# Kernel optimization log

Measured on AMD Instinct MI355X. Metric: run time of the kernel, lower is better.

## Reference

```python
import jax, jax.numpy as jnp
import numpy as np
import math

B, S, D = 2, 2048, 2048
H = 16
DK = D // H  # 128
DFF = 5440
THETA = 10000.0
EPS = 1e-5


def setup_inputs() -> dict:
    key = jax.random.key(0)
    ks = jax.random.split(key, 9)
    sc = 0.02
    return {
        "x": jax.random.normal(ks[0], (B, S, D), jnp.float32),
        "wq": jax.random.normal(ks[1], (D, D), jnp.float32) * sc,
        "wk": jax.random.normal(ks[2], (D, D), jnp.float32) * sc,
        "wv": jax.random.normal(ks[3], (D, D), jnp.float32) * sc,
        "wo": jax.random.normal(ks[4], (D, D), jnp.float32) * sc,
        "w1": jax.random.normal(ks[5], (DFF, D), jnp.float32) * sc,
        "w2": jax.random.normal(ks[6], (D, DFF), jnp.float32) * sc,
        "w3": jax.random.normal(ks[7], (DFF, D), jnp.float32) * sc,
        "g_attn": jnp.ones((D,), jnp.float32),
        "g_ffn": jnp.ones((D,), jnp.float32),
    }


def _rmsnorm(x, g):
    xf = x.astype(jnp.float32)
    rms = jnp.sqrt(jnp.mean(xf * xf, axis=-1, keepdims=True) + EPS)
    return (xf / rms * g).astype(x.dtype)


def _rope(x):
    # x: (B, H, S, DK)
    pair = jnp.arange(0, DK, 2, dtype=jnp.float32)
    inv_freq = 1.0 / (THETA ** (pair / DK))            # (DK/2,)
    pos = jnp.arange(S, dtype=jnp.float32)
    ang = pos[:, None] * inv_freq[None, :]             # (S, DK/2)
    cos, sin = jnp.cos(ang), jnp.sin(ang)
    xe, xo = x[..., 0::2], x[..., 1::2]
    oe = xe * cos - xo * sin
    oo = xe * sin + xo * cos
    # interleave even/odd back
    out = jnp.stack([oe, oo], axis=-1).reshape(x.shape)
    return out


def reference(x, wq, wk, wv, wo, w1, w2, w3, g_attn, g_ffn):
    # --- attention sublayer ---
    h = _rmsnorm(x, g_attn)
    q = (h @ wq.T).reshape(B, S, H, DK).transpose(0, 2, 1, 3)
    k = (h @ wk.T).reshape(B, S, H, DK).transpose(0, 2, 1, 3)
    v = (h @ wv.T).reshape(B, S, H, DK).transpose(0, 2, 1, 3)
    q = _rope(q)
    k = _rope(k)
    scores = jnp.einsum("bhqd,bhkd->bhqk", q, k) / math.sqrt(DK)
    causal = jnp.tril(jnp.ones((S, S), dtype=bool))
    scores = jnp.where(causal, scores, jnp.finfo(scores.dtype).min)
    attn = jax.nn.softmax(scores, axis=-1)
    o = jnp.einsum("bhqk,bhkd->bhqd", attn, v)
    o = o.transpose(0, 2, 1, 3).reshape(B, S, D)
    x = x + o @ wo.T
    # --- SwiGLU FFN sublayer ---
    h = _rmsnorm(x, g_ffn)
    a = h @ w1.T
    gate = a * jax.nn.sigmoid(a)
    ff = (gate * (h @ w3.T)) @ w2.T
    return x + ff
```

## Files before the change

### kernel.cpp

```cpp
#include <hip/hip_runtime.h>
#include <cstdint>
#include <cstddef>

typedef float  f32x4  __attribute__((ext_vector_type(4)));
typedef __bf16 bf16x8 __attribute__((ext_vector_type(8)));
typedef unsigned short u16x8 __attribute__((ext_vector_type(8)));
typedef unsigned short u16x4 __attribute__((ext_vector_type(4)));
typedef unsigned short u16x2 __attribute__((ext_vector_type(2)));

#define DEV static __device__ __forceinline__

DEV unsigned short f2bfu(float f) { __bf16 b = (__bf16)f; return __builtin_bit_cast(unsigned short, b); }
DEV float bfu2f(unsigned short u) { return (float)__builtin_bit_cast(__bf16, u); }
DEV bf16x8 ldb8(const void* p) { return __builtin_bit_cast(bf16x8, *(const u16x8*)p); }
DEV float fexp(float x) { return __builtin_amdgcn_exp2f(x * 1.44269504f); }

DEV f32x4 mfma16(bf16x8 a, bf16x8 b, f32x4 c) {
  return __builtin_amdgcn_mfma_f32_16x16x32_bf16(a, b, c, 0, 0, 0);
}

DEV void gload16(const void* g, void* l) {
  __builtin_amdgcn_global_load_lds((const unsigned int*)g, (unsigned int*)l, 16, 0, 0);
}

#define FENCE() asm volatile("" ::: "memory")
#define LGKM0() asm volatile("s_waitcnt lgkmcnt(0)" ::: "memory")
#define VMC8()  asm volatile("s_waitcnt vmcnt(8)" ::: "memory")
#define VMC4()  asm volatile("s_waitcnt vmcnt(4)" ::: "memory")
#define VMC0()  asm volatile("s_waitcnt vmcnt(0)" ::: "memory")
#define SBAR()  __builtin_amdgcn_s_barrier()
#define SCH0()  __builtin_amdgcn_sched_barrier(0)
#define PRIO1() __builtin_amdgcn_s_setprio(1)
#define PRIO0() __builtin_amdgcn_s_setprio(0)

__global__ __launch_bounds__(256) void conv_cat3(
    const float* __restrict__ s0, const float* __restrict__ s1,
    const float* __restrict__ s2, unsigned short* __restrict__ d)
{
  size_t i = (size_t)blockIdx.x * 256 + threadIdx.x;
  size_t e = i * 4;
  const float* s = e < 4194304 ? s0 : (e < 8388608 ? s1 : s2);
  f32x4 v = *(const f32x4*)(s + (e & 4194303));
  u16x4 o = { f2bfu(v.x), f2bfu(v.y), f2bfu(v.z), f2bfu(v.w) };
  *(u16x4*)(d + e) = o;
}

__global__ __launch_bounds__(256) void conv_plain(
    const float* __restrict__ s, unsigned short* __restrict__ d)
{
  size_t e = ((size_t)blockIdx.x * 256 + threadIdx.x) * 4;
  f32x4 v = *(const f32x4*)(s + e);
  u16x4 o = { f2bfu(v.x), f2bfu(v.y), f2bfu(v.z), f2bfu(v.w) };
  *(u16x4*)(d + e) = o;
}

__global__ __launch_bounds__(256) void conv_w13(
    const float* __restrict__ w1, const float* __restrict__ w3,
    unsigned short* __restrict__ d)
{
  size_t i = (size_t)blockIdx.x * 256 + threadIdx.x;
  size_t e = i * 4;
  if (e >= 22544384ull) return;
  int n = (int)(e >> 11), kc = (int)(e & 2047);
  int grp = n >> 4;
  int srcrow = (grp >> 1) * 16 + (n & 15);
  if (srcrow >= 5440) srcrow = 5439;
  const float* s = (grp & 1) ? w3 : w1;
  size_t off = (size_t)srcrow * 2048 + kc;
  f32x4 v = *(const f32x4*)(s + off);
  u16x4 o = { f2bfu(v.x), f2bfu(v.y), f2bfu(v.z), f2bfu(v.w) };
  *(u16x4*)(d + e) = o;
}

template<int EPI>
__global__ __launch_bounds__(256) void gemm_p(
    const unsigned short* __restrict__ A, const unsigned short* __restrict__ B,
    void* __restrict__ D0, void* __restrict__ D1, void* __restrict__ D2,
    const float* __restrict__ auxf, const float* __restrict__ cosT,
    const float* __restrict__ sinT, int M, int N, int K)
{
  __shared__ __align__(16) char Asb[4 * 8192];
  __shared__ __align__(16) char Bsb[4 * 8192];

  const int tid = threadIdx.x, lane = tid & 63, w = tid >> 6;
  const int wr = w >> 1, wc = w & 1, l15 = lane & 15, lg = lane >> 4;
  const int m0 = blockIdx.x * 128, n0 = blockIdx.y * 128;

  const int srow = tid >> 2, s4 = tid & 3;
  const int s4s = s4 ^ ((srow >> 1) & 3);
  const unsigned short* As0 = A + (size_t)(m0 + srow) * K + s4s * 8;
  const unsigned short* As1 = A + (size_t)(m0 + 64 + srow) * K + s4s * 8;
  const unsigned short* Bs0 = B + (size_t)(n0 + srow) * K + s4s * 8;
  const unsigned short* Bs1 = B + (size_t)(n0 + 64 + srow) * K + s4s * 8;
  const int dst0 = tid * 16, dst1 = 4096 + tid * 16;

#define STG_A(kh, db, kt) do { char* r = Asb + ((kh)*2+(db))*8192;            \
    gload16(As0 + (size_t)(kt)*64 + (kh)*32, r + dst0);                        \
    gload16(As1 + (size_t)(kt)*64 + (kh)*32, r + dst1); } while(0)
#define STG_B(kh, db, kt) do { char* r = Bsb + ((kh)*2+(db))*8192;            \
    gload16(Bs0 + (size_t)(kt)*64 + (kh)*32, r + dst0);                        \
    gload16(Bs1 + (size_t)(kt)*64 + (kh)*32, r + dst1); } while(0)

  f32x4 zero = {0.f, 0.f, 0.f, 0.f};
  f32x4 acc[4][4];
#pragma unroll
  for (int i = 0; i < 4; i++)
#pragma unroll
    for (int j = 0; j < 4; j++) acc[i][j] = zero;

  int aro[4], bro[4];
#pragma unroll
  for (int mi = 0; mi < 4; mi++) {
    int row = wr * 64 + mi * 16 + l15;
    aro[mi] = row * 64 + ((lg ^ ((row >> 1) & 3)) << 4);
  }
#pragma unroll
  for (int ni = 0; ni < 4; ni++) {
    int row = wc * 64 + ni * 16 + l15;
    bro[ni] = row * 64 + ((lg ^ ((row >> 1) & 3)) << 4);
  }

  const int nkt = K >> 6;

  STG_A(0, 0, 0); STG_B(0, 0, 0); STG_A(1, 0, 0); STG_B(1, 0, 0);

  for (int t = 0; t < nkt; ++t) {
    const int db = t & 1, dn = db ^ 1;
    const bool pf = (t + 1) < nkt;
    const char* Ar0 = Asb + (0 * 2 + db) * 8192;
    const char* Br0 = Bsb + (0 * 2 + db) * 8192;
    const char* Ar1 = Asb + (1 * 2 + db) * 8192;
    const char* Br1 = Bsb + (1 * 2 + db) * 8192;

    VMC4(); FENCE(); SBAR();
    bf16x8 af[4], bfr[4];
#pragma unroll
    for (int ni = 0; ni < 4; ni++) bfr[ni] = ldb8(Br0 + bro[ni]);
#pragma unroll
    for (int mi = 0; mi < 4; mi++) af[mi] = ldb8(Ar0 + aro[mi]);
    if (pf) { STG_A(0, dn, t + 1); STG_B(0, dn, t + 1); }
    LGKM0(); SCH0();
    PRIO1();
#pragma unroll
    for (int mi = 0; mi < 4; mi++)
#pragma unroll
      for (int ni = 0; ni < 4; ni++)
        acc[mi][ni] = mfma16(af[mi], bfr[ni], acc[mi][ni]);
    PRIO0();

    if (pf) { VMC4(); } else { VMC0(); }
    FENCE(); SBAR();
#pragma unroll
    for (int ni = 0; ni < 4; ni++) bfr[ni] = ldb8(Br1 + bro[ni]);
#pragma unroll
    for (int mi = 0; mi < 4; mi++) af[mi] = ldb8(Ar1 + aro[mi]);
    if (pf) { STG_A(1, dn, t + 1); STG_B(1, dn, t + 1); }
    LGKM0(); SCH0();
    PRIO1();
#pragma unroll
    for (int mi = 0; mi < 4; mi++)
#pragma unroll
      for (int ni = 0; ni < 4; ni++)
        acc[mi][ni] = mfma16(af[mi], bfr[ni], acc[mi][ni]);
    PRIO0();
  }
#undef STG_A
#undef STG_B

  if constexpr (EPI == 0) {
    unsigned short* qd = (unsigned short*)D0;
    unsigned short* kd = (unsigned short*)D1;
    unsigned short* vd = (unsigned short*)D2;
#pragma unroll
    for (int mi = 0; mi < 4; mi++) {
#pragma unroll
      for (int ni = 0; ni < 4; ni++) {
        int col = n0 + wc * 64 + ni * 16 + l15;
#pragma unroll
        for (int r = 0; r < 4; r++) {
          int row = m0 + wr * 64 + mi * 16 + lg * 4 + r;
          float v = acc[mi][ni][r];
          if (col < 4096) {
            int d = col & 127, pi = d >> 1, sp = row & 2047;
            float c = cosT[sp * 64 + pi], s = sinT[sp * 64 + pi];
            float part = __shfl_xor(v, 1);
            float res = (d & 1) ? (part * s + v * c) : (v * c - part * s);
            unsigned short* dst = (col < 2048) ? qd : kd;
            dst[(size_t)row * 2048 + (col & 2047)] = f2bfu(res);
          } else {
            int vdc = col - 4096;
            vd[((size_t)((row >> 11) * 2048 + vdc)) * 2048 + (row & 2047)] = f2bfu(v);
          }
        }
      }
    }
  } else {
    float* O = (float*)D0;
#pragma unroll
    for (int mi = 0; mi < 4; mi++)
#pragma unroll
      for (int ni = 0; ni < 4; ni++) {
        int col = n0 + wc * 64 + ni * 16 + l15;
#pragma unroll
        for (int r = 0; r < 4; r++) {
          int row = m0 + wr * 64 + mi * 16 + lg * 4 + r;
          size_t ix = (size_t)row * 2048 + col;
          if constexpr (EPI == 1) O[ix] = auxf[ix] + acc[mi][ni][r];
          else                    O[ix] = O[ix] + acc[mi][ni][r];
        }
      }
  }
}

template<int EPI>
__global__ __launch_bounds__(512, 1) void gemm8v2(
    const unsigned short* __restrict__ A, const unsigned short* __restrict__ B,
    void* __restrict__ D0, int M, int N, int K)
{
  __shared__ __align__(16) char Asb[4 * 16384];
  __shared__ __align__(16) char Bsb[4 * 16384];

  const int tid = threadIdx.x, lane = tid & 63, w = tid >> 6;
  const int wm = w >> 2, wn = w & 3;
  const int l15 = lane & 15, lg = lane >> 4;

  const int nwg = gridDim.x, chunk = nwg >> 3;
  const int wg = (blockIdx.x & 7) * chunk + (blockIdx.x >> 3);
  const int MT = M >> 8;
  const int mt = wg % MT, nt = wg / MT;
  const int m0 = mt * 256, n0 = nt * 256;

  const int srow = tid >> 2;
  const int s4   = tid & 3;
  const int s4s  = s4 ^ ((srow >> 1) & 3);
  const unsigned short* As0 = A + (size_t)(m0 + srow) * K + s4s * 8;
  const unsigned short* As1 = A + (size_t)(m0 + 128 + srow) * K + s4s * 8;
  const unsigned short* Bs0 = B + (size_t)(n0 + srow) * K + s4s * 8;
  const unsigned short* Bs1 = B + (size_t)(n0 + 128 + srow) * K + s4s * 8;
  const int dst0 = tid * 16, dst1 = 8192 + tid * 16;

#define STAGE_A(kh, db, kt) do { char* rgn = Asb + ((kh)*2+(db))*16384;       \
    gload16(As0 + (size_t)(kt)*64 + (kh)*32, rgn + dst0);                      \
    gload16(As1 + (size_t)(kt)*64 + (kh)*32, rgn + dst1); } while(0)
#define STAGE_B(kh, db, kt) do { char* rgn = Bsb + ((kh)*2+(db))*16384;       \
    gload16(Bs0 + (size_t)(kt)*64 + (kh)*32, rgn + dst0);                      \
    gload16(Bs1 + (size_t)(kt)*64 + (kh)*32, rgn + dst1); } while(0)

  f32x4 zero = {0.f, 0.f, 0.f, 0.f};
  f32x4 acc[8][4];
#pragma unroll
  for (int i = 0; i < 8; i++)
#pragma unroll
    for (int j = 0; j < 4; j++) acc[i][j] = zero;

  int aro[8], bro[4];
#pragma unroll
  for (int mi = 0; mi < 8; mi++) {
    int row = wm * 128 + mi * 16 + l15;
    aro[mi] = row * 64 + ((lg ^ ((row >> 1) & 3)) << 4);
  }
#pragma unroll
  for (int ni = 0; ni < 4; ni++) {
    int row = wn * 64 + ni * 16 + l15;
    bro[ni] = row * 64 + ((lg ^ ((row >> 1) & 3)) << 4);
  }

  const int nkt = K >> 6;

  STAGE_A(0, 0, 0); STAGE_B(0, 0, 0); STAGE_A(1, 0, 0); STAGE_B(1, 0, 0);

  for (int t = 0; t < nkt; ++t) {
    const int db = t & 1, dn = db ^ 1;
    const bool pf = (t + 1) < nkt;
    const char* Ar0 = Asb + (0 * 2 + db) * 16384;
    const char* Br0 = Bsb + (0 * 2 + db) * 16384;
    const char* Ar1 = Asb + (1 * 2 + db) * 16384;
    const char* Br1 = Bsb + (1 * 2 + db) * 16384;

    VMC4(); FENCE(); SBAR();
    bf16x8 bfr[4], af[4];
#pragma unroll
    for (int ni = 0; ni < 4; ni++) bfr[ni] = ldb8(Br0 + bro[ni]);
#pragma unroll
    for (int mi = 0; mi < 4; mi++) af[mi] = ldb8(Ar0 + aro[mi]);
    if (pf) STAGE_A(0, dn, t + 1);
    LGKM0(); SCH0();
    PRIO1();
#pragma unroll
    for (int mi = 0; mi < 4; mi++)
#pragma unroll
      for (int ni = 0; ni < 4; ni++)
        acc[mi][ni] = mfma16(af[mi], bfr[ni], acc[mi][ni]);
    PRIO0();

    bf16x8 ag[4];
#pragma unroll
    for (int mi = 0; mi < 4; mi++) ag[mi] = ldb8(Ar0 + aro[mi + 4]);
    if (pf) STAGE_B(0, dn, t + 1);
    LGKM0(); SCH0();
    PRIO1();
#pragma unroll
    for (int mi = 0; mi < 4; mi++)
#pragma unroll
      for (int ni = 0; ni < 4; ni++)
        acc[mi + 4][ni] = mfma16(ag[mi], bfr[ni], acc[mi + 4][ni]);
    PRIO0();

    if (pf) { VMC4(); } else { VMC0(); }
    FENCE(); SBAR();
#pragma unroll
    for (int ni = 0; ni < 4; ni++) bfr[ni] = ldb8(Br1 + bro[ni]);
#pragma unroll
    for (int mi = 0; mi < 4; mi++) af[mi] = ldb8(Ar1 + aro[mi]);
    if (pf) STAGE_A(1, dn, t + 1);
    LGKM0(); SCH0();
    PRIO1();
#pragma unroll
    for (int mi = 0; mi < 4; mi++)
#pragma unroll
      for (int ni = 0; ni < 4; ni++)
        acc[mi][ni] = mfma16(af[mi], bfr[ni], acc[mi][ni]);
    PRIO0();

#pragma unroll
    for (int mi = 0; mi < 4; mi++) ag[mi] = ldb8(Ar1 + aro[mi + 4]);
    if (pf) STAGE_B(1, dn, t + 1);
    LGKM0(); SCH0();
    PRIO1();
#pragma unroll
    for (int mi = 0; mi < 4; mi++)
#pragma unroll
      for (int ni = 0; ni < 4; ni++)
        acc[mi + 4][ni] = mfma16(ag[mi], bfr[ni], acc[mi + 4][ni]);
    PRIO0();
  }
#undef STAGE_A
#undef STAGE_B

  if constexpr (EPI == 2) {
    unsigned short* G = (unsigned short*)D0;
#pragma unroll
    for (int mi = 0; mi < 8; mi++)
#pragma unroll
      for (int nj = 0; nj < 2; nj++) {
        int outc = (nt * 8 + wn * 2 + nj) * 16 + l15;
        if (outc >= 5440) continue;
#pragma unroll
        for (int r = 0; r < 4; r++) {
          int row = m0 + wm * 128 + mi * 16 + lg * 4 + r;
          float a = acc[mi][2 * nj][r];
          float c = acc[mi][2 * nj + 1][r];
          float sg = a / (1.0f + fexp(-a));
          G[(size_t)row * 5440 + outc] = f2bfu(sg * c);
        }
      }
  }
}

__global__ __launch_bounds__(256) void rmsnorm_k(
    const float* __restrict__ x, const float* __restrict__ g,
    unsigned short* __restrict__ out)
{
  int row = blockIdx.x, t = threadIdx.x;
  const float* xr = x + (size_t)row * 2048;
  f32x4 v0 = ((const f32x4*)xr)[t];
  f32x4 v1 = ((const f32x4*)xr)[t + 256];
  float ss = v0.x*v0.x + v0.y*v0.y + v0.z*v0.z + v0.w*v0.w
           + v1.x*v1.x + v1.y*v1.y + v1.z*v1.z + v1.w*v1.w;
  __shared__ float red[256];
  red[t] = ss; __syncthreads();
  for (int sh = 128; sh > 0; sh >>= 1) {
    if (t < sh) red[t] += red[t + sh];
    __syncthreads();
  }
  float rinv = rsqrtf(red[0] * (1.0f / 2048.0f) + 1e-5f);
  f32x4 g0 = ((const f32x4*)g)[t];
  f32x4 g1 = ((const f32x4*)g)[t + 256];
  u16x4 o0 = { f2bfu(v0.x*rinv*g0.x), f2bfu(v0.y*rinv*g0.y),
               f2bfu(v0.z*rinv*g0.z), f2bfu(v0.w*rinv*g0.w) };
  u16x4 o1 = { f2bfu(v1.x*rinv*g1.x), f2bfu(v1.y*rinv*g1.y),
               f2bfu(v1.z*rinv*g1.z), f2bfu(v1.w*rinv*g1.w) };
  *(u16x4*)(out + (size_t)row * 2048 + t * 4) = o0;
  *(u16x4*)(out + (size_t)row * 2048 + 1024 + t * 4) = o1;
}

__global__ __launch_bounds__(256) void rope_tab(float* __restrict__ cosT,
                                                float* __restrict__ sinT)
{
  int idx = blockIdx.x * 256 + threadIdx.x;
  int s = idx >> 6, p = idx & 63;
  float ang = (float)s * powf(10000.0f, -(float)p / 64.0f);
  cosT[idx] = cosf(ang);
  sinT[idx] = sinf(ang);
}

__global__ __launch_bounds__(256) void attn_fwd(
    const unsigned short* __restrict__ q, const unsigned short* __restrict__ k,
    const unsigned short* __restrict__ vt, unsigned short* __restrict__ o)
{
  const int S = 2048, Dm = 2048;
  const int tid  = threadIdx.x;
  const int lane = tid & 63;
  const int w    = tid >> 6;
  const int hh   = blockIdx.y, b = blockIdx.z;
  const int l15  = lane & 15, lg = lane >> 4;
  const float SCALE = 0.08838834764831845f;

  __shared__ __align__(16) char Ksb[2][16384];
  __shared__ __align__(16) char Vsb[2][16384];
  __shared__ __align__(16) unsigned short Ps[4][16 * 76];

  const unsigned short* kg = k  + ((size_t)(b * S)) * Dm + hh * 128;
  const unsigned short* vg = vt + ((size_t)((b * 16 + hh) * 128)) * S;

  const int krs = tid >> 4, ksp = (tid & 15) ^ (krs & 7);
  const int vrs = tid >> 3, vsp = (tid & 7) ^ (vrs & 7);

#define STAGE_KV(j, buf) do {                                                  \
    int kv_ = (j) * 64;                                                        \
    _Pragma("unroll")                                                          \
    for (int rr = 0; rr < 4; rr++)                                             \
      gload16(kg + (size_t)(kv_ + rr * 16 + krs) * 2048 + ksp * 8,             \
              Ksb[buf] + (rr * 256 + tid) * 16);                               \
    _Pragma("unroll")                                                          \
    for (int rr = 0; rr < 4; rr++)                                             \
      gload16(vg + (size_t)(rr * 32 + vrs) * 2048 + kv_ + vsp * 8,             \
              Vsb[buf] + (rr * 256 + tid) * 16);                               \
  } while (0)

  for (int half = 0; half < 2; ++half) {
    const int qt = half ? (31 - blockIdx.x) : blockIdx.x;
    const int r0 = qt * 64;
    const int myq = r0 + w * 16 + l15;

    STAGE_KV(0, 0);

    bf16x8 qf[4];
    size_t qbase = ((size_t)(b * S + r0 + w * 16 + l15)) * Dm + hh * 128 + lg * 8;
#pragma unroll
    for (int kk = 0; kk < 4; kk++) qf[kk] = ldb8(q + qbase + kk * 32);

    f32x4 zero = {0.f, 0.f, 0.f, 0.f};
    f32x4 accO[8];
#pragma unroll
    for (int dt = 0; dt < 8; dt++) accO[dt] = zero;
    float mrun = -1e30f, lrun = 0.f;

    int ntile = qt + 1;
    for (int j = 0; j < ntile; ++j) {
      int kv0 = j * 64;
      const int db = j & 1;
      const bool pf = (j + 1) < ntile;
      if (pf) STAGE_KV(j + 1, db ^ 1);
      if (pf) { VMC8(); } else { VMC0(); }
      FENCE(); SBAR();

      const char* Ks = Ksb[db];
      const char* Vs = Vsb[db];

      f32x4 sfr[4];
#pragma unroll
      for (int sv = 0; sv < 4; sv++) sfr[sv] = zero;
#pragma unroll
      for (int kk = 0; kk < 4; kk++) {
#pragma unroll
        for (int sv = 0; sv < 4; sv++) {
          int row = sv * 16 + l15;
          int boff = (row * 256 + kk * 64 + lg * 16) ^ ((row & 7) << 4);
          bf16x8 kf = ldb8(Ks + boff);
          sfr[sv] = mfma16(kf, qf[kk], sfr[sv]);
        }
      }

      float tmax = -1e30f;
#pragma unroll
      for (int sv = 0; sv < 4; sv++)
#pragma unroll
        for (int r = 0; r < 4; r++) {
          int kvv = kv0 + sv * 16 + lg * 4 + r;
          float val = (kvv <= myq) ? sfr[sv][r] * SCALE : -1e30f;
          sfr[sv][r] = val;
          tmax = fmaxf(tmax, val);
        }
      tmax = fmaxf(tmax, __shfl_xor(tmax, 16));
      tmax = fmaxf(tmax, __shfl_xor(tmax, 32));
      float mnew = fmaxf(mrun, tmax);
      float alpha = fexp(mrun - mnew);
      float psum = 0.f;
#pragma unroll
      for (int sv = 0; sv < 4; sv++)
#pragma unroll
        for (int r = 0; r < 4; r++) {
          float pvv = fexp(sfr[sv][r] - mnew);
          sfr[sv][r] = pvv;
          psum += pvv;
        }
      psum += __shfl_xor(psum, 16);
      psum += __shfl_xor(psum, 32);
      lrun = lrun * alpha + psum;
      mrun = mnew;

      float al[4];
#pragma unroll
      for (int r = 0; r < 4; r++)
        al[r] = __shfl(alpha, (lane & 48) + lg * 4 + r);
#pragma unroll
      for (int dt = 0; dt < 8; dt++) {
        f32x4 t = accO[dt];
        t[0] *= al[0]; t[1] *= al[1]; t[2] *= al[2]; t[3] *= al[3];
        accO[dt] = t;
      }

#pragma unroll
      for (int sv = 0; sv < 4; sv++) {
        u16x2 lo = { f2bfu(sfr[sv][0]), f2bfu(sfr[sv][1]) };
        u16x2 hi = { f2bfu(sfr[sv][2]), f2bfu(sfr[sv][3]) };
        *(u16x2*)&Ps[w][l15 * 76 + sv * 16 + lg * 4]     = lo;
        *(u16x2*)&Ps[w][l15 * 76 + sv * 16 + lg * 4 + 2] = hi;
      }

      bf16x8 pa[2];
      pa[0] = ldb8(&Ps[w][l15 * 76 + lg * 8]);
      pa[1] = ldb8(&Ps[w][l15 * 76 + 32 + lg * 8]);
#pragma unroll
      for (int dt = 0; dt < 8; dt++) {
#pragma unroll
        for (int kk = 0; kk < 2; kk++) {
          int row = dt * 16 + l15;
          int boff = (row * 128 + kk * 64 + lg * 16) ^ ((row & 7) << 4);
          bf16x8 vb = ldb8(Vs + boff);
          accO[dt] = mfma16(pa[kk], vb, accO[dt]);
        }
      }
      FENCE(); SBAR();
    }

    float lf[4];
#pragma unroll
    for (int r = 0; r < 4; r++)
      lf[r] = __shfl(lrun, (lane & 48) + lg * 4 + r);
#pragma unroll
    for (int dt = 0; dt < 8; dt++) {
#pragma unroll
      for (int r = 0; r < 4; r++) {
        int qr = r0 + w * 16 + lg * 4 + r;
        o[((size_t)(b * S + qr)) * Dm + hh * 128 + dt * 16 + l15] =
            f2bfu(accO[dt][r] / lf[r]);
      }
    }
  }
#undef STAGE_KV
}

extern "C" void kernel_launch(void* const* d_in, const int* in_sizes, int n_in,
                              void* d_out, int out_size, void* d_ws, size_t ws_size,
                              hipStream_t stream)
{
  const float* x      = (const float*)d_in[0];
  const float* wq     = (const float*)d_in[1];
  const float* wk     = (const float*)d_in[2];
  const float* wv     = (const float*)d_in[3];
  const float* wo     = (const float*)d_in[4];
  const float* w1     = (const float*)d_in[5];
  const float* w2     = (const float*)d_in[6];
  const float* w3     = (const float*)d_in[7];
  const float* g_attn = (const float*)d_in[8];
  const float* g_ffn  = (const float*)d_in[9];
  float* out = (float*)d_out;

  unsigned short* W = (unsigned short*)d_ws;
  unsigned short* h_bf    = W;
  unsigned short* q_bf    = W + 8388608ull;
  unsigned short* k_bf    = W + 16777216ull;
  unsigned short* vt_bf   = W + 25165824ull;
  unsigned short* o_bf    = W + 33554432ull;
  unsigned short* wqkv_bf = W + 41943040ull;
  unsigned short* wo_bf   = W + 54525952ull;
  unsigned short* w13_bf  = W + 58720256ull;
  unsigned short* w2_bf   = W + 81264640ull;
  unsigned short* a1_bf   = q_bf;
  float* cosT = (float*)o_bf;
  float* sinT = cosT + 131072;

  dim3 blk(256);
  rope_tab<<<512, blk, 0, stream>>>(cosT, sinT);
  conv_cat3<<<12288, blk, 0, stream>>>(wq, wk, wv, wqkv_bf);
  conv_plain<<<4096, blk, 0, stream>>>(wo, wo_bf);
  conv_w13<<<22016, blk, 0, stream>>>(w1, w3, w13_bf);
  conv_plain<<<10880, blk, 0, stream>>>(w2, w2_bf);

  rmsnorm_k<<<4096, blk, 0, stream>>>(x, g_attn, h_bf);

  gemm_p<0><<<dim3(32, 48), blk, 0, stream>>>(h_bf, wqkv_bf, q_bf, k_bf, vt_bf,
                                              nullptr, cosT, sinT, 4096, 6144, 2048);

  attn_fwd<<<dim3(16, 16, 2), blk, 0, stream>>>(q_bf, k_bf, vt_bf, o_bf);

  gemm_p<1><<<dim3(32, 16), blk, 0, stream>>>(o_bf, wo_bf, out, nullptr, nullptr,
                                              x, nullptr, nullptr, 4096, 2048, 2048);
  rmsnorm_k<<<4096, blk, 0, stream>>>(out, g_ffn, h_bf);

  gemm8v2<2><<<dim3(688), dim3(512), 0, stream>>>(h_bf, w13_bf, a1_bf, 4096, 11008, 2048);

  gemm_p<3><<<dim3(32, 16), blk, 0, stream>>>(a1_bf, w2_bf, out, nullptr, nullptr,
                                              nullptr, nullptr, nullptr, 4096, 2048, 5440);
}
```

Measured before the change: 655.9 us.

## Restructure causal attention: 32-key tiles, one q-tile per block, lazy rescale

```diff
diff --git a/kernel.cpp b/kernel.cpp
--- a/kernel.cpp
+++ b/kernel.cpp
@@ -14,6 +14,7 @@
 DEV float bfu2f(unsigned short u) { return (float)__builtin_bit_cast(__bf16, u); }
 DEV bf16x8 ldb8(const void* p) { return __builtin_bit_cast(bf16x8, *(const u16x8*)p); }
 DEV float fexp(float x) { return __builtin_amdgcn_exp2f(x * 1.44269504f); }
+DEV float fexp2(float x) { return __builtin_amdgcn_exp2f(x); }
 
 DEV f32x4 mfma16(bf16x8 a, bf16x8 b, f32x4 c) {
   return __builtin_amdgcn_mfma_f32_16x16x32_bf16(a, b, c, 0, 0, 0);
@@ -25,7 +26,6 @@
 
 #define FENCE() asm volatile("" ::: "memory")
 #define LGKM0() asm volatile("s_waitcnt lgkmcnt(0)" ::: "memory")
-#define VMC8()  asm volatile("s_waitcnt vmcnt(8)" ::: "memory")
 #define VMC4()  asm volatile("s_waitcnt vmcnt(4)" ::: "memory")
 #define VMC0()  asm volatile("s_waitcnt vmcnt(0)" ::: "memory")
 #define SBAR()  __builtin_amdgcn_s_barrier()
@@ -404,102 +404,92 @@
   const int w    = tid >> 6;
   const int hh   = blockIdx.y, b = blockIdx.z;
   const int l15  = lane & 15, lg = lane >> 4;
-  const float SCALE = 0.08838834764831845f;
-
-  __shared__ __align__(16) char Ksb[2][16384];
-  __shared__ __align__(16) char Vsb[2][16384];
-  __shared__ __align__(16) unsigned short Ps[4][16 * 76];
+  const float C = 0.08838834764831845f * 1.44269504f;
+
+  __shared__ __align__(16) char Ksb[2][8192];
+  __shared__ __align__(16) char Vsb[2][8192];
+  __shared__ __align__(16) unsigned short Ps[4][16 * 40];
 
   const unsigned short* kg = k  + ((size_t)(b * S)) * Dm + hh * 128;
   const unsigned short* vg = vt + ((size_t)((b * 16 + hh) * 128)) * S;
 
   const int krs = tid >> 4, ksp = (tid & 15) ^ (krs & 7);
-  const int vrs = tid >> 3, vsp = (tid & 7) ^ (vrs & 7);
+  const int vrs = tid >> 2, vsp = (tid & 3) ^ (vrs & 3);
 
 #define STAGE_KV(j, buf) do {                                                  \
-    int kv_ = (j) * 64;                                                        \
+    int kv_ = (j) * 32;                                                        \
     _Pragma("unroll")                                                          \
-    for (int rr = 0; rr < 4; rr++)                                             \
+    for (int rr = 0; rr < 2; rr++)                                             \
       gload16(kg + (size_t)(kv_ + rr * 16 + krs) * 2048 + ksp * 8,             \
               Ksb[buf] + (rr * 256 + tid) * 16);                               \
     _Pragma("unroll")                                                          \
-    for (int rr = 0; rr < 4; rr++)                                             \
-      gload16(vg + (size_t)(rr * 32 + vrs) * 2048 + kv_ + vsp * 8,             \
+    for (int rr = 0; rr < 2; rr++)                                             \
+      gload16(vg + (size_t)(rr * 64 + vrs) * 2048 + kv_ + vsp * 8,             \
               Vsb[buf] + (rr * 256 + tid) * 16);                               \
   } while (0)
 
-  for (int half = 0; half < 2; ++half) {
-    const int qt = half ? (31 - blockIdx.x) : blockIdx.x;
-    const int r0 = qt * 64;
-    const int myq = r0 + w * 16 + l15;
-
-    STAGE_KV(0, 0);
-
-    bf16x8 qf[4];
-    size_t qbase = ((size_t)(b * S + r0 + w * 16 + l15)) * Dm + hh * 128 + lg * 8;
-#pragma unroll
-    for (int kk = 0; kk < 4; kk++) qf[kk] = ldb8(q + qbase + kk * 32);
-
-    f32x4 zero = {0.f, 0.f, 0.f, 0.f};
-    f32x4 accO[8];
-#pragma unroll
-    for (int dt = 0; dt < 8; dt++) accO[dt] = zero;
-    float mrun = -1e30f, lrun = 0.f;
-
-    int ntile = qt + 1;
-    for (int j = 0; j < ntile; ++j) {
-      int kv0 = j * 64;
-      const int db = j & 1;
-      const bool pf = (j + 1) < ntile;
-      if (pf) STAGE_KV(j + 1, db ^ 1);
-      if (pf) { VMC8(); } else { VMC0(); }
-      FENCE(); SBAR();
-
-      const char* Ks = Ksb[db];
-      const char* Vs = Vsb[db];
-
-      f32x4 sfr[4];
-#pragma unroll
-      for (int sv = 0; sv < 4; sv++) sfr[sv] = zero;
-#pragma unroll
-      for (int kk = 0; kk < 4; kk++) {
-#pragma unroll
-        for (int sv = 0; sv < 4; sv++) {
-          int row = sv * 16 + l15;
-          int boff = (row * 256 + kk * 64 + lg * 16) ^ ((row & 7) << 4);
-          bf16x8 kf = ldb8(Ks + boff);
-          sfr[sv] = mfma16(kf, qf[kk], sfr[sv]);
-        }
+  const int qt = 31 - blockIdx.x;
+  const int r0 = qt * 64;
+  const int myq = r0 + w * 16 + l15;
+
+  STAGE_KV(0, 0);
+
+  bf16x8 qf[4];
+  size_t qbase = ((size_t)(b * S + r0 + w * 16 + l15)) * Dm + hh * 128 + lg * 8;
+#pragma unroll
+  for (int kk = 0; kk < 4; kk++) qf[kk] = ldb8(q + qbase + kk * 32);
+
+  f32x4 zero = {0.f, 0.f, 0.f, 0.f};
+  f32x4 accO[8];
+#pragma unroll
+  for (int dt = 0; dt < 8; dt++) accO[dt] = zero;
+  float mrun = -1e30f, lrun = 0.f;
+
+  const int ntile = 2 * qt + 2;
+  for (int j = 0; j < ntile; ++j) {
+    int kv0 = j * 32;
+    const int db = j & 1;
+    const bool pf = (j + 1) < ntile;
+    if (pf) STAGE_KV(j + 1, db ^ 1);
+    if (pf) { VMC4(); } else { VMC0(); }
+    FENCE(); SBAR();
+
+    const char* Ks = Ksb[db];
+    const char* Vs = Vsb[db];
+
+    f32x4 sfr[2];
+    sfr[0] = zero; sfr[1] = zero;
+    PRIO1();
+#pragma unroll
+    for (int kk = 0; kk < 4; kk++) {
+#pragma unroll
+      for (int sv = 0; sv < 2; sv++) {
+        int row = sv * 16 + l15;
+        int boff = (row * 256 + kk * 64 + lg * 16) ^ ((row & 7) << 4);
+        bf16x8 kf = ldb8(Ks + boff);
+        sfr[sv] = mfma16(kf, qf[kk], sfr[sv]);
       }
-
-      float tmax = -1e30f;
-#pragma unroll
-      for (int sv = 0; sv < 4; sv++)
-#pragma unroll
-        for (int r = 0; r < 4; r++) {
-          int kvv = kv0 + sv * 16 + lg * 4 + r;
-          float val = (kvv <= myq) ? sfr[sv][r] * SCALE : -1e30f;
-          sfr[sv][r] = val;
-          tmax = fmaxf(tmax, val);
-        }
-      tmax = fmaxf(tmax, __shfl_xor(tmax, 16));
-      tmax = fmaxf(tmax, __shfl_xor(tmax, 32));
+    }
+    PRIO0();
+
+    float tmax = -1e30f;
+#pragma unroll
+    for (int sv = 0; sv < 2; sv++)
+#pragma unroll
+      for (int r = 0; r < 4; r++) {
+        int kvv = kv0 + sv * 16 + lg * 4 + r;
+        float val = (kvv <= myq) ? sfr[sv][r] : -1e30f;
+        sfr[sv][r] = val;
+        tmax = fmaxf(tmax, val);
+      }
+    tmax = fmaxf(tmax, __shfl_xor(tmax, 16));
+    tmax = fmaxf(tmax, __shfl_xor(tmax, 32));
+
+    if (!__all(tmax <= mrun + 64.0f)) {
       float mnew = fmaxf(mrun, tmax);
-      float alpha = fexp(mrun - mnew);
-      float psum = 0.f;
-#pragma unroll
-      for (int sv = 0; sv < 4; sv++)
-#pragma unroll
-        for (int r = 0; r < 4; r++) {
-          float pvv = fexp(sfr[sv][r] - mnew);
-          sfr[sv][r] = pvv;
-          psum += pvv;
-        }
-      psum += __shfl_xor(psum, 16);
-      psum += __shfl_xor(psum, 32);
-      lrun = lrun * alpha + psum;
+      float alpha = fexp2((mrun - mnew) * C);
+      lrun *= alpha;
       mrun = mnew;
-
       float al[4];
 #pragma unroll
       for (int r = 0; r < 4; r++)
@@ -510,43 +500,53 @@
         t[0] *= al[0]; t[1] *= al[1]; t[2] *= al[2]; t[3] *= al[3];
         accO[dt] = t;
       }
-
-#pragma unroll
-      for (int sv = 0; sv < 4; sv++) {
-        u16x2 lo = { f2bfu(sfr[sv][0]), f2bfu(sfr[sv][1]) };
-        u16x2 hi = { f2bfu(sfr[sv][2]), f2bfu(sfr[sv][3]) };
-        *(u16x2*)&Ps[w][l15 * 76 + sv * 16 + lg * 4]     = lo;
-        *(u16x2*)&Ps[w][l15 * 76 + sv * 16 + lg * 4 + 2] = hi;
+    }
+
+    float psum = 0.f;
+#pragma unroll
+    for (int sv = 0; sv < 2; sv++)
+#pragma unroll
+      for (int r = 0; r < 4; r++) {
+        float pvv = fexp2((sfr[sv][r] - mrun) * C);
+        sfr[sv][r] = pvv;
+        psum += pvv;
       }
-
-      bf16x8 pa[2];
-      pa[0] = ldb8(&Ps[w][l15 * 76 + lg * 8]);
-      pa[1] = ldb8(&Ps[w][l15 * 76 + 32 + lg * 8]);
-#pragma unroll
-      for (int dt = 0; dt < 8; dt++) {
-#pragma unroll
-        for (int kk = 0; kk < 2; kk++) {
-          int row = dt * 16 + l15;
-          int boff = (row * 128 + kk * 64 + lg * 16) ^ ((row & 7) << 4);
-          bf16x8 vb = ldb8(Vs + boff);
-          accO[dt] = mfma16(pa[kk], vb, accO[dt]);
-        }
-      }
-      FENCE(); SBAR();
+    psum += __shfl_xor(psum, 16);
+    psum += __shfl_xor(psum, 32);
+    lrun += psum;
+
+#pragma unroll
+    for (int sv = 0; sv < 2; sv++) {
+      u16x2 lo = { f2bfu(sfr[sv][0]), f2bfu(sfr[sv][1]) };
+      u16x2 hi = { f2bfu(sfr[sv][2]), f2bfu(sfr[sv][3]) };
+      *(u16x2*)&Ps[w][l15 * 40 + sv * 16 + lg * 4]     = lo;
+      *(u16x2*)&Ps[w][l15 * 40 + sv * 16 + lg * 4 + 2] = hi;
     }
 
-    float lf[4];
-#pragma unroll
-    for (int r = 0; r < 4; r++)
-      lf[r] = __shfl(lrun, (lane & 48) + lg * 4 + r);
+    bf16x8 pa = ldb8(&Ps[w][l15 * 40 + lg * 8]);
+    PRIO1();
 #pragma unroll
     for (int dt = 0; dt < 8; dt++) {
-#pragma unroll
-      for (int r = 0; r < 4; r++) {
-        int qr = r0 + w * 16 + lg * 4 + r;
-        o[((size_t)(b * S + qr)) * Dm + hh * 128 + dt * 16 + l15] =
-            f2bfu(accO[dt][r] / lf[r]);
-      }
+      int row = dt * 16 + l15;
+      int boff = (row * 64 + lg * 16) ^ ((row & 3) << 4);
+      bf16x8 vb = ldb8(Vs + boff);
+      accO[dt] = mfma16(pa, vb, accO[dt]);
+    }
+    PRIO0();
+    FENCE(); SBAR();
+  }
+
+  float lf[4];
+#pragma unroll
+  for (int r = 0; r < 4; r++)
+    lf[r] = __shfl(lrun, (lane & 48) + lg * 4 + r);
+#pragma unroll
+  for (int dt = 0; dt < 8; dt++) {
+#pragma unroll
+    for (int r = 0; r < 4; r++) {
+      int qr = r0 + w * 16 + lg * 4 + r;
+      o[((size_t)(b * S + qr)) * Dm + hh * 128 + dt * 16 + l15] =
+          f2bfu(accO[dt][r] / lf[r]);
     }
   }
 #undef STAGE_KV
@@ -594,7 +594,7 @@
   gemm_p<0><<<dim3(32, 48), blk, 0, stream>>>(h_bf, wqkv_bf, q_bf, k_bf, vt_bf,
                                               nullptr, cosT, sinT, 4096, 6144, 2048);
 
-  attn_fwd<<<dim3(16, 16, 2), blk, 0, stream>>>(q_bf, k_bf, vt_bf, o_bf);
+  attn_fwd<<<dim3(32, 16, 2), blk, 0, stream>>>(q_bf, k_bf, vt_bf, o_bf);
 
   gemm_p<1><<<dim3(32, 16), blk, 0, stream>>>(o_bf, wo_bf, out, nullptr, nullptr,
                                               x, nullptr, nullptr, 4096, 2048, 2048);
```

Result: slower. 734.9 us (+12.0%).
